# Kernel optimization log

Measured on AMD Instinct MI355X. Metric: run time of the kernel, lower is better.

The kernel has to match this reference:

```python
import jax, jax.numpy as jnp
import numpy as np

TOP_K = 2


def setup_inputs() -> dict:
    key = jax.random.key(0)
    k1, k2, k3, k4 = jax.random.split(key, 4)
    B, S, D, F, E = 4, 2048, 1024, 4096, 8
    return {
        "inputs": jax.random.normal(k1, (B, S, D), dtype=jnp.float32),
        "gate_w": jax.random.normal(k2, (D, E), dtype=jnp.float32) * 0.02,
        "w1": jax.random.normal(k3, (E, D, F), dtype=jnp.float32) * 0.02,
        "w2": jax.random.normal(k4, (E, F, D), dtype=jnp.float32) * 0.02,
    }


def reference(inputs, gate_w, w1, w2):
    # gate logits: [B, S, E]
    gate_logits = jnp.einsum("bsd,de->bse", inputs, gate_w)
    E = gate_logits.shape[-1]

    # router KL loss (matches F.kl_div(log(mean_prob), uniform, reduction='batchmean')):
    # kl = sum(u * (log u - log p_mean)) / E   (batchmean divides by first dim = E)
    gate_prob = jax.nn.softmax(gate_logits.astype(jnp.float32), axis=-1).astype(inputs.dtype)
    mean_prob = gate_prob.mean(axis=(0, 1))  # [E]
    u = jnp.full((E,), 1.0 / E, dtype=mean_prob.dtype)
    kl_loss = jnp.sum(u * (jnp.log(u) - jnp.log(mean_prob))) / E

    # top-k routing
    weights, selected = jax.lax.top_k(gate_logits, TOP_K)  # [B,S,k]
    prob = jax.nn.softmax(weights.astype(jnp.float32), axis=-1).astype(inputs.dtype)

    # combine weight per expert: [B,S,E]; zero for unselected experts
    onehot = jax.nn.one_hot(selected, E, dtype=prob.dtype)  # [B,S,k,E]
    combine = jnp.einsum("bsk,bske->bse", prob, onehot)

    results = jnp.zeros_like(inputs)
    for i in range(E):  # fixed small loop over experts
        h = jax.nn.silu(jnp.einsum("bsd,df->bsf", inputs, w1[i]))
        out = jnp.einsum("bsf,fd->bsd", h, w2[i])
        results = results + combine[..., i : i + 1] * out
    return (results, kl_loss)
```

## Files before the change

kernel.cpp:

```cpp
#include <hip/hip_runtime.h>
#include <hip/hip_bf16.h>
#include <cstdint>


#define N_TOK 8192
#define D_DIM 1024
#define F_DIM 4096
#define N_EXP 8
#define MB_MAX 72

#define CNT_OFF   0u
#define HOFF_OFF  64u
#define NMB_OFF   104u
#define ZPG_OFF   128u
#define MBE_OFF   256u
#define MBB_OFF   896u
#define PSUM_OFF  1536u
#define LIST_OFF  67072u
#define COEF_OFF  329216u
#define H1_OFF    1048576ull
#define XBF_OFF   1048576ull
#define W1T_OFF   18874368ull
#define W2T_OFF   (W1T_OFF + 67108864ull)
#define H2_OFF    (W2T_OFF + 67108864ull)
#define FULL_WS   (H2_OFF + 18432ull * 4096ull * 2ull)

typedef __attribute__((ext_vector_type(8))) short short8;
typedef __attribute__((ext_vector_type(4))) float f32x4;
typedef __attribute__((ext_vector_type(4))) float float4v;
typedef __attribute__((ext_vector_type(2))) unsigned int u32x2;

__device__ __forceinline__ unsigned short f2bf(float x) {
  unsigned int u = __float_as_uint(x);
  unsigned int r = (u + 0x7fffu + ((u >> 16) & 1u)) >> 16;
  return (unsigned short)r;
}

__device__ __forceinline__ void gload16(const void* g, void* l) {
  __builtin_amdgcn_global_load_lds(
      (const __attribute__((address_space(1))) void*)g,
      (__attribute__((address_space(3))) void*)l, 16, 0, 0);
}

__global__ void router_kernel(const float* __restrict__ x,
                              const float* __restrict__ gw,
                              int* __restrict__ cnt, int* __restrict__ list,
                              float* __restrict__ coef,
                              float* __restrict__ psum,
                              unsigned short* __restrict__ xbf) {
  const int wave = threadIdx.x >> 6;
  const int lane = threadIdx.x & 63;
  const int t = blockIdx.x * 4 + wave;

  __shared__ float bps[N_EXP];
  if (threadIdx.x < N_EXP) bps[threadIdx.x] = 0.f;
  __syncthreads();

  float lg[8] = {0.f, 0.f, 0.f, 0.f, 0.f, 0.f, 0.f, 0.f};
  const float* xr = x + (size_t)t * D_DIM;
  unsigned short* xbr = xbf + (size_t)t * D_DIM;
#pragma unroll
  for (int i = 0; i < 16; ++i) {
    int d = lane + i * 64;
    float xv = xr[d];
    xbr[d] = f2bf(xv);
    float4v w0 = *(const float4v*)(gw + d * 8);
    float4v w1 = *(const float4v*)(gw + d * 8 + 4);
    lg[0] = fmaf(xv, w0.x, lg[0]); lg[1] = fmaf(xv, w0.y, lg[1]);
    lg[2] = fmaf(xv, w0.z, lg[2]); lg[3] = fmaf(xv, w0.w, lg[3]);
    lg[4] = fmaf(xv, w1.x, lg[4]); lg[5] = fmaf(xv, w1.y, lg[5]);
    lg[6] = fmaf(xv, w1.z, lg[6]); lg[7] = fmaf(xv, w1.w, lg[7]);
  }
#pragma unroll
  for (int m = 32; m; m >>= 1) {
#pragma unroll
    for (int e = 0; e < 8; ++e) lg[e] += __shfl_xor(lg[e], m);
  }

  if (lane == 0) {
    float mx = lg[0];
#pragma unroll
    for (int e = 1; e < 8; ++e) mx = fmaxf(mx, lg[e]);
    float p[8], s = 0.f;
#pragma unroll
    for (int e = 0; e < 8; ++e) { p[e] = expf(lg[e] - mx); s += p[e]; }
    float inv = 1.f / s;
#pragma unroll
    for (int e = 0; e < 8; ++e) atomicAdd(&bps[e], p[e] * inv);

    int i0 = 0;
#pragma unroll
    for (int e = 1; e < 8; ++e) if (lg[e] > lg[i0]) i0 = e;
    int i1 = (i0 == 0) ? 1 : 0;
#pragma unroll
    for (int e = 0; e < 8; ++e) if (e != i1 && e != i0 && lg[e] > lg[i1]) i1 = e;
    float p0 = 1.f / (1.f + expf(lg[i1] - lg[i0]));
    float p1 = 1.f - p0;
    int s0 = atomicAdd(&cnt[i0], 1);
    list[i0 * N_TOK + s0] = t; coef[i0 * N_TOK + s0] = p0;
    int s1 = atomicAdd(&cnt[i1], 1);
    list[i1 * N_TOK + s1] = t; coef[i1 * N_TOK + s1] = p1;
  }
  __syncthreads();
  if (threadIdx.x < 8) psum[blockIdx.x * 8 + threadIdx.x] = bps[threadIdx.x];
}

__global__ void prefix_kernel(const int* __restrict__ cnt, int* __restrict__ hoff,
                              int* __restrict__ mbe, int* __restrict__ mbb,
                              int* __restrict__ nmb, int g) {
  if (threadIdx.x == 0) {
    int o = 0, gmb = 0;
    for (int e = 0; e < 8; ++e) {
      hoff[e] = o;
      int nb = (cnt[e] + g - 1) / g;
      for (int m = 0; m < nb; ++m) { mbe[gmb] = e; mbb[gmb] = m; ++gmb; }
      o += nb * g;
    }
    hoff[8] = o;
    *nmb = gmb;
  }
}

__global__ void kl_kernel(const float* __restrict__ psum, float* __restrict__ out_kl) {
  __shared__ float s[8];
  if (threadIdx.x < 8) s[threadIdx.x] = 0.f;
  __syncthreads();
  float loc[8] = {0.f, 0.f, 0.f, 0.f, 0.f, 0.f, 0.f, 0.f};
  for (int r = threadIdx.x; r < 2048; r += 256) {
#pragma unroll
    for (int e = 0; e < 8; ++e) loc[e] += psum[r * 8 + e];
  }
#pragma unroll
  for (int e = 0; e < 8; ++e) atomicAdd(&s[e], loc[e]);
  __syncthreads();
  if (threadIdx.x == 0) {
    float kl = 0.f;
#pragma unroll
    for (int e = 0; e < 8; ++e) {
      float mean = s[e] / 8192.f;
      kl += (logf(0.125f) - logf(mean));
    }
    out_kl[0] = kl * (0.125f * 0.125f);
  }
}

__global__ __launch_bounds__(256) void wtrans_kernel(
    const float* __restrict__ w, unsigned short* __restrict__ wt, int K, int N) {
  const int e = blockIdx.z;
  const int n0 = blockIdx.x * 64, k0 = blockIdx.y * 64;
  __shared__ float t[64][65];
  const float* we = w + (size_t)e * K * N;
  const int nl = threadIdx.x & 63;
  const int kl4 = threadIdx.x >> 6;
#pragma unroll
  for (int r = 0; r < 16; ++r) {
    int kl = r * 4 + kl4;
    t[kl][nl] = we[(size_t)(k0 + kl) * N + n0 + nl];
  }
  __syncthreads();
  unsigned short* wte = wt + (size_t)e * K * N;
  const int kp = (threadIdx.x & 31) * 2;
  const int nl8 = threadIdx.x >> 5;
#pragma unroll
  for (int r = 0; r < 8; ++r) {
    int n = r * 8 + nl8;
    unsigned int pk = (unsigned int)f2bf(t[kp][n]) |
                      ((unsigned int)f2bf(t[kp + 1][n]) << 16);
    *(unsigned int*)(wte + (size_t)(n0 + n) * K + k0 + kp) = pk;
  }
}

__device__ __forceinline__ short8 ld_frag(const unsigned short* base, int row_base,
                                          int k_base, int lane) {
  int row = row_base + (lane & 15);
  int byte = (row * 128 + (k_base + ((lane >> 4) << 3)) * 2) ^ ((row & 7) << 4);
  return *(const short8*)((const char*)base + byte);
}

__global__ __launch_bounds__(512, 2) void gemm1_v6(
    const unsigned short* __restrict__ xbf, const unsigned short* __restrict__ w1t,
    const int* __restrict__ cnt, const int* __restrict__ hoff,
    const int* __restrict__ mbe, const int* __restrict__ mbb,
    const int* __restrict__ nmb,
    const int* __restrict__ list, const unsigned short* __restrict__ zpage,
    unsigned short* __restrict__ h) {
  const int mb = blockIdx.y;
  if (mb >= *nmb) return;
  const int e = mbe[mb], mblk = mbb[mb], nblk = blockIdx.x;
  const int c = cnt[e];
  const int tid = threadIdx.x, lane = tid & 63, wave = tid >> 6;
  const int wm = (wave >> 1) * 64, wn = (wave & 1) * 64;

  __shared__ unsigned short As[256 * 64];
  __shared__ unsigned short Bs[128 * 64];

  const int rowb = tid >> 3;
  const int sw = (((tid & 7) ^ (rowb & 7)) << 4);
  const char* asrc[4]; int astep[4];
  const char* bsrc[2];
#pragma unroll
  for (int i = 0; i < 4; ++i) {
    int row = i * 64 + rowb;
    int slot = mblk * 256 + row;
    if (slot < c) {
      int tok = list[e * N_TOK + slot];
      asrc[i] = (const char*)(xbf + (size_t)tok * D_DIM) + sw;
      astep[i] = 128;
    } else {
      asrc[i] = (const char*)zpage + sw;
      astep[i] = 0;
    }
  }
#pragma unroll
  for (int i = 0; i < 2; ++i) {
    int row = i * 64 + rowb;
    bsrc[i] = (const char*)(w1t + ((size_t)e * F_DIM + nblk * 128 + row) * D_DIM) + sw;
  }

  f32x4 acc[4][4];
#pragma unroll
  for (int i = 0; i < 4; ++i)
#pragma unroll
    for (int j = 0; j < 4; ++j) acc[i][j] = f32x4{0.f, 0.f, 0.f, 0.f};

  for (int kc = 0; kc < 16; ++kc) {
    __syncthreads();
#pragma unroll
    for (int i = 0; i < 4; ++i) {
      gload16(asrc[i], (char*)As + i * 8192 + tid * 16);
      asrc[i] += astep[i];
    }
#pragma unroll
    for (int i = 0; i < 2; ++i) {
      gload16(bsrc[i], (char*)Bs + i * 8192 + tid * 16);
      bsrc[i] += 128;
    }
    __syncthreads();
#pragma unroll
    for (int ks = 0; ks < 2; ++ks) {
      short8 af[4], bb[4];
#pragma unroll
      for (int mf = 0; mf < 4; ++mf) af[mf] = ld_frag(As, wm + mf * 16, ks * 32, lane);
#pragma unroll
      for (int nf = 0; nf < 4; ++nf) bb[nf] = ld_frag(Bs, wn + nf * 16, ks * 32, lane);
#pragma unroll
      for (int mf = 0; mf < 4; ++mf)
#pragma unroll
        for (int nf = 0; nf < 4; ++nf)
          acc[mf][nf] = __builtin_amdgcn_mfma_f32_16x16x32_bf16(
              af[mf], bb[nf], acc[mf][nf], 0, 0, 0);
    }
  }

  const int hbase = hoff[e] + mblk * 256;
#pragma unroll
  for (int mf = 0; mf < 4; ++mf)
#pragma unroll
    for (int nf = 0; nf < 4; ++nf)
#pragma unroll
      for (int r = 0; r < 4; ++r) {
        float v = acc[mf][nf][r];
        v = v / (1.f + __expf(-v));
        int row = wm + mf * 16 + ((lane >> 4) << 2) + r;
        int col = nblk * 128 + wn + nf * 16 + (lane & 15);
        h[(size_t)(hbase + row) * F_DIM + col] = f2bf(v);
      }
}

__global__ __launch_bounds__(512, 2) void gemm2_v6(
    const unsigned short* __restrict__ h, const unsigned short* __restrict__ w2t,
    const int* __restrict__ cnt, const int* __restrict__ hoff,
    const int* __restrict__ mbe, const int* __restrict__ mbb,
    const int* __restrict__ nmb,
    const int* __restrict__ list, const float* __restrict__ coef,
    float* __restrict__ out) {
  const int mb = blockIdx.y;
  if (mb >= *nmb) return;
  const int e = mbe[mb], mblk = mbb[mb], nblk = blockIdx.x;
  const int c = cnt[e];
  const int kofs = blockIdx.z * 2048;
  const int tid = threadIdx.x, lane = tid & 63, wave = tid >> 6;
  const int wm = (wave >> 1) * 64, wn = (wave & 1) * 64;

  __shared__ unsigned short As[256 * 64];
  __shared__ unsigned short Bs[128 * 64];

  const int rowb = tid >> 3;
  const int sw = (((tid & 7) ^ (rowb & 7)) << 4);
  const int hbase = hoff[e] + mblk * 256;
  const char* asrc[4];
  const char* bsrc[2];
#pragma unroll
  for (int i = 0; i < 4; ++i) {
    int row = i * 64 + rowb;
    asrc[i] = (const char*)(h + (size_t)(hbase + row) * F_DIM + kofs) + sw;
  }
#pragma unroll
  for (int i = 0; i < 2; ++i) {
    int row = i * 64 + rowb;
    bsrc[i] = (const char*)(w2t + ((size_t)e * D_DIM + nblk * 128 + row) * F_DIM + kofs) + sw;
  }

  f32x4 acc[4][4];
#pragma unroll
  for (int i = 0; i < 4; ++i)
#pragma unroll
    for (int j = 0; j < 4; ++j) acc[i][j] = f32x4{0.f, 0.f, 0.f, 0.f};

  for (int kc = 0; kc < 32; ++kc) {
    __syncthreads();
#pragma unroll
    for (int i = 0; i < 4; ++i) {
      gload16(asrc[i], (char*)As + i * 8192 + tid * 16);
      asrc[i] += 128;
    }
#pragma unroll
    for (int i = 0; i < 2; ++i) {
      gload16(bsrc[i], (char*)Bs + i * 8192 + tid * 16);
      bsrc[i] += 128;
    }
    __syncthreads();
#pragma unroll
    for (int ks = 0; ks < 2; ++ks) {
      short8 af[4], bb[4];
#pragma unroll
      for (int mf = 0; mf < 4; ++mf) af[mf] = ld_frag(As, wm + mf * 16, ks * 32, lane);
#pragma unroll
      for (int nf = 0; nf < 4; ++nf) bb[nf] = ld_frag(Bs, wn + nf * 16, ks * 32, lane);
#pragma unroll
      for (int mf = 0; mf < 4; ++mf)
#pragma unroll
        for (int nf = 0; nf < 4; ++nf)
          acc[mf][nf] = __builtin_amdgcn_mfma_f32_16x16x32_bf16(
              af[mf], bb[nf], acc[mf][nf], 0, 0, 0);
    }
  }

#pragma unroll
  for (int mf = 0; mf < 4; ++mf) {
#pragma unroll
    for (int r = 0; r < 4; ++r) {
      int slot = mblk * 256 + wm + mf * 16 + ((lane >> 4) << 2) + r;
      if (slot < c) {
        int tok = list[e * N_TOK + slot];
        float cf = coef[e * N_TOK + slot];
#pragma unroll
        for (int nf = 0; nf < 4; ++nf) {
          int col = nblk * 128 + wn + nf * 16 + (lane & 15);
          unsafeAtomicAdd(&out[(size_t)tok * D_DIM + col], cf * acc[mf][nf][r]);
        }
      }
    }
  }
}

__global__ __launch_bounds__(256) void gemm1_v1(
    const float* __restrict__ x, const float* __restrict__ w1,
    const int* __restrict__ cnt, const int* __restrict__ hoff,
    const int* __restrict__ list, unsigned short* __restrict__ h) {
  const int e = blockIdx.z, mblk = blockIdx.y, nblk = blockIdx.x;
  const int c = cnt[e];
  if (mblk * 128 >= c) return;
  const int tid = threadIdx.x, lane = tid & 63, wave = tid >> 6;
  const int wm = (wave >> 1) * 64, wn = (wave & 1) * 64;

  __shared__ unsigned short At[128 * 64];
  __shared__ unsigned short Bt[128 * 64];
  __shared__ int toks[128];
  if (tid < 128) {
    int slot = mblk * 128 + tid;
    toks[tid] = (slot < c) ? list[e * N_TOK + slot] : -1;
  }
  __syncthreads();

  f32x4 acc[4][4];
#pragma unroll
  for (int i = 0; i < 4; ++i)
#pragma unroll
    for (int j = 0; j < 4; ++j) acc[i][j] = f32x4{0.f, 0.f, 0.f, 0.f};

  const float* w1e = w1 + (size_t)e * D_DIM * F_DIM;
  for (int kc = 0; kc < 16; ++kc) {
    __syncthreads();
#pragma unroll
    for (int it = 0; it < 8; ++it) {
      int lin = it * 256 + tid;
      int row = lin >> 4, c4 = lin & 15;
      int tok = toks[row];
      unsigned int lo = 0u, hi = 0u;
      if (tok >= 0) {
        float4v f = *(const float4v*)(x + (size_t)tok * D_DIM + kc * 64 + c4 * 4);
        lo = (unsigned int)f2bf(f.x) | ((unsigned int)f2bf(f.y) << 16);
        hi = (unsigned int)f2bf(f.z) | ((unsigned int)f2bf(f.w) << 16);
      }
      int byte = (row * 128 + c4 * 8) ^ ((row & 7) << 4);
      *(u32x2*)((char*)At + byte) = u32x2{lo, hi};
    }
#pragma unroll
    for (int it = 0; it < 16; ++it) {
      int lin = it * 256 + tid;
      int f_loc = lin & 127, dp = lin >> 7;
      int d = kc * 64 + dp * 2;
      const float* src = w1e + (size_t)d * F_DIM + nblk * 128 + f_loc;
      unsigned int pk = (unsigned int)f2bf(src[0]) |
                        ((unsigned int)f2bf(src[F_DIM]) << 16);
      int byte = (f_loc * 128 + dp * 4) ^ ((f_loc & 7) << 4);
      *(unsigned int*)((char*)Bt + byte) = pk;
    }
    __syncthreads();
#pragma unroll
    for (int ks = 0; ks < 2; ++ks) {
      short8 af[4], bb[4];
#pragma unroll
      for (int mf = 0; mf < 4; ++mf) af[mf] = ld_frag(At, wm + mf * 16, ks * 32, lane);
#pragma unroll
      for (int nf = 0; nf < 4; ++nf) bb[nf] = ld_frag(Bt, wn + nf * 16, ks * 32, lane);
#pragma unroll
      for (int mf = 0; mf < 4; ++mf)
#pragma unroll
        for (int nf = 0; nf < 4; ++nf)
          acc[mf][nf] = __builtin_amdgcn_mfma_f32_16x16x32_bf16(
              af[mf], bb[nf], acc[mf][nf], 0, 0, 0);
    }
  }

  const int hbase = hoff[e] + mblk * 128;
#pragma unroll
  for (int mf = 0; mf < 4; ++mf)
#pragma unroll
    for (int nf = 0; nf < 4; ++nf)
#pragma unroll
      for (int r = 0; r < 4; ++r) {
        float v = acc[mf][nf][r];
        v = v / (1.f + __expf(-v));
        int row = wm + mf * 16 + ((lane >> 4) << 2) + r;
        int col = nblk * 128 + wn + nf * 16 + (lane & 15);
        h[(size_t)(hbase + row) * F_DIM + col] = f2bf(v);
      }
}

__global__ __launch_bounds__(256) void gemm2_v1(
    const unsigned short* __restrict__ h, const float* __restrict__ w2,
    const int* __restrict__ cnt, const int* __restrict__ hoff,
    const int* __restrict__ list, const float* __restrict__ coef,
    float* __restrict__ out) {
  const int e = blockIdx.z, mblk = blockIdx.y, nblk = blockIdx.x;
  const int c = cnt[e];
  if (mblk * 128 >= c) return;
  const int tid = threadIdx.x, lane = tid & 63, wave = tid >> 6;
  const int wm = (wave >> 1) * 64, wn = (wave & 1) * 64;

  __shared__ unsigned short At[128 * 64];
  __shared__ unsigned short Bt[128 * 64];

  f32x4 acc[4][4];
#pragma unroll
  for (int i = 0; i < 4; ++i)
#pragma unroll
    for (int j = 0; j < 4; ++j) acc[i][j] = f32x4{0.f, 0.f, 0.f, 0.f};

  const int hbase = hoff[e] + mblk * 128;
  const float* w2e = w2 + (size_t)e * F_DIM * D_DIM;
  for (int kc = 0; kc < 64; ++kc) {
    __syncthreads();
#pragma unroll
    for (int it = 0; it < 8; ++it) {
      int lin = it * 256 + tid;
      int row = lin >> 4, c4 = lin & 15;
      u32x2 v = *(const u32x2*)(h + (size_t)(hbase + row) * F_DIM + kc * 64 + c4 * 4);
      int byte = (row * 128 + c4 * 8) ^ ((row & 7) << 4);
      *(u32x2*)((char*)At + byte) = v;
    }
#pragma unroll
    for (int it = 0; it < 16; ++it) {
      int lin = it * 256 + tid;
      int dcol = lin & 127, kp = lin >> 7;
      int k = kc * 64 + kp * 2;
      const float* src = w2e + (size_t)k * D_DIM + nblk * 128 + dcol;
      unsigned int pk = (unsigned int)f2bf(src[0]) |
                        ((unsigned int)f2bf(src[D_DIM]) << 16);
      int byte = (dcol * 128 + kp * 4) ^ ((dcol & 7) << 4);
      *(unsigned int*)((char*)Bt + byte) = pk;
    }
    __syncthreads();
#pragma unroll
    for (int ks = 0; ks < 2; ++ks) {
      short8 af[4], bb[4];
#pragma unroll
      for (int mf = 0; mf < 4; ++mf) af[mf] = ld_frag(At, wm + mf * 16, ks * 32, lane);
#pragma unroll
      for (int nf = 0; nf < 4; ++nf) bb[nf] = ld_frag(Bt, wn + nf * 16, ks * 32, lane);
#pragma unroll
      for (int mf = 0; mf < 4; ++mf)
#pragma unroll
        for (int nf = 0; nf < 4; ++nf)
          acc[mf][nf] = __builtin_amdgcn_mfma_f32_16x16x32_bf16(
              af[mf], bb[nf], acc[mf][nf], 0, 0, 0);
    }
  }

#pragma unroll
  for (int mf = 0; mf < 4; ++mf) {
#pragma unroll
    for (int r = 0; r < 4; ++r) {
      int slot = mblk * 128 + wm + mf * 16 + ((lane >> 4) << 2) + r;
      if (slot < c) {
        int tok = list[e * N_TOK + slot];
        float cf = coef[e * N_TOK + slot];
#pragma unroll
        for (int nf = 0; nf < 4; ++nf) {
          int col = nblk * 128 + wn + nf * 16 + (lane & 15);
          unsafeAtomicAdd(&out[(size_t)tok * D_DIM + col], cf * acc[mf][nf][r]);
        }
      }
    }
  }
}

extern "C" void kernel_launch(void* const* d_in, const int* in_sizes, int n_in,
                              void* d_out, int out_size, void* d_ws, size_t ws_size,
                              hipStream_t stream) {
  const float* x = (const float*)d_in[0];
  const float* gw = (const float*)d_in[1];
  const float* w1 = (const float*)d_in[2];
  const float* w2 = (const float*)d_in[3];
  float* out = (float*)d_out;
  char* ws = (char*)d_ws;

  int* cnt = (int*)(ws + CNT_OFF);
  int* hoff = (int*)(ws + HOFF_OFF);
  int* nmb = (int*)(ws + NMB_OFF);
  int* mbe = (int*)(ws + MBE_OFF);
  int* mbb = (int*)(ws + MBB_OFF);
  float* psum = (float*)(ws + PSUM_OFF);
  int* list = (int*)(ws + LIST_OFF);
  float* coef = (float*)(ws + COEF_OFF);
  unsigned short* xbf = (unsigned short*)(ws + XBF_OFF);

  const bool full = (ws_size >= FULL_WS);

  hipMemsetAsync(d_ws, 0, PSUM_OFF + 2048 * 8 * 4, stream);
  hipMemsetAsync(d_out, 0, (size_t)out_size * 4, stream);

  router_kernel<<<2048, 256, 0, stream>>>(x, gw, cnt, list, coef, psum, xbf);
  prefix_kernel<<<1, 64, 0, stream>>>(cnt, hoff, mbe, mbb, nmb, full ? 256 : 128);
  kl_kernel<<<1, 256, 0, stream>>>(psum, out + 8388608);

  if (full) {
    unsigned short* w1t = (unsigned short*)(ws + W1T_OFF);
    unsigned short* w2t = (unsigned short*)(ws + W2T_OFF);
    unsigned short* h = (unsigned short*)(ws + H2_OFF);
    const unsigned short* zpage = (const unsigned short*)(ws + ZPG_OFF);

    wtrans_kernel<<<dim3(64, 16, 8), 256, 0, stream>>>(w1, w1t, 1024, 4096);
    wtrans_kernel<<<dim3(16, 64, 8), 256, 0, stream>>>(w2, w2t, 4096, 1024);
    gemm1_v6<<<dim3(32, MB_MAX), 512, 0, stream>>>(xbf, w1t, cnt, hoff, mbe, mbb,
                                                   nmb, list, zpage, h);
    gemm2_v6<<<dim3(8, MB_MAX, 2), 512, 0, stream>>>(h, w2t, cnt, hoff, mbe, mbb,
                                                     nmb, list, coef, out);
  } else {
    unsigned short* h = (unsigned short*)(ws + H1_OFF);
    gemm1_v1<<<dim3(32, 64, 8), 256, 0, stream>>>(x, w1, cnt, hoff, list, h);
    gemm2_v1<<<dim3(8, 64, 8), 256, 0, stream>>>(h, w2, cnt, hoff, list, coef, out);
  }
}
```

Measured before the change: 878.3 us.

## Enlarge MoE expert GEMM tiles to 256x256 and reorder grid to m-block-major

```diff
diff --git a/kernel.cpp b/kernel.cpp
--- a/kernel.cpp
+++ b/kernel.cpp
@@ -177,27 +177,27 @@
   return *(const short8*)((const char*)base + byte);
 }
 
-__global__ __launch_bounds__(512, 2) void gemm1_v6(
+__global__ __launch_bounds__(512, 2) void gemm1_v7(
     const unsigned short* __restrict__ xbf, const unsigned short* __restrict__ w1t,
     const int* __restrict__ cnt, const int* __restrict__ hoff,
     const int* __restrict__ mbe, const int* __restrict__ mbb,
     const int* __restrict__ nmb,
     const int* __restrict__ list, const unsigned short* __restrict__ zpage,
     unsigned short* __restrict__ h) {
-  const int mb = blockIdx.y;
+  const int mb = blockIdx.x;
   if (mb >= *nmb) return;
-  const int e = mbe[mb], mblk = mbb[mb], nblk = blockIdx.x;
+  const int e = mbe[mb], mblk = mbb[mb], nblk = blockIdx.y;
   const int c = cnt[e];
   const int tid = threadIdx.x, lane = tid & 63, wave = tid >> 6;
-  const int wm = (wave >> 1) * 64, wn = (wave & 1) * 64;
+  const int wm = (wave >> 2) * 128, wn = (wave & 3) * 64;
 
   __shared__ unsigned short As[256 * 64];
-  __shared__ unsigned short Bs[128 * 64];
+  __shared__ unsigned short Bs[256 * 64];
 
   const int rowb = tid >> 3;
   const int sw = (((tid & 7) ^ (rowb & 7)) << 4);
   const char* asrc[4]; int astep[4];
-  const char* bsrc[2];
+  const char* bsrc[4];
 #pragma unroll
   for (int i = 0; i < 4; ++i) {
     int row = i * 64 + rowb;
@@ -210,16 +210,12 @@
       asrc[i] = (const char*)zpage + sw;
       astep[i] = 0;
     }
-  }
-#pragma unroll
-  for (int i = 0; i < 2; ++i) {
-    int row = i * 64 + rowb;
-    bsrc[i] = (const char*)(w1t + ((size_t)e * F_DIM + nblk * 128 + row) * D_DIM) + sw;
-  }
-
-  f32x4 acc[4][4];
-#pragma unroll
-  for (int i = 0; i < 4; ++i)
+    bsrc[i] = (const char*)(w1t + ((size_t)e * F_DIM + nblk * 256 + row) * D_DIM) + sw;
+  }
+
+  f32x4 acc[8][4];
+#pragma unroll
+  for (int i = 0; i < 8; ++i)
 #pragma unroll
     for (int j = 0; j < 4; ++j) acc[i][j] = f32x4{0.f, 0.f, 0.f, 0.f};
 
@@ -229,22 +225,19 @@
     for (int i = 0; i < 4; ++i) {
       gload16(asrc[i], (char*)As + i * 8192 + tid * 16);
       asrc[i] += astep[i];
-    }
-#pragma unroll
-    for (int i = 0; i < 2; ++i) {
       gload16(bsrc[i], (char*)Bs + i * 8192 + tid * 16);
       bsrc[i] += 128;
     }
     __syncthreads();
 #pragma unroll
     for (int ks = 0; ks < 2; ++ks) {
-      short8 af[4], bb[4];
-#pragma unroll
-      for (int mf = 0; mf < 4; ++mf) af[mf] = ld_frag(As, wm + mf * 16, ks * 32, lane);
+      short8 af[8], bb[4];
+#pragma unroll
+      for (int mf = 0; mf < 8; ++mf) af[mf] = ld_frag(As, wm + mf * 16, ks * 32, lane);
 #pragma unroll
       for (int nf = 0; nf < 4; ++nf) bb[nf] = ld_frag(Bs, wn + nf * 16, ks * 32, lane);
 #pragma unroll
-      for (int mf = 0; mf < 4; ++mf)
+      for (int mf = 0; mf < 8; ++mf)
 #pragma unroll
         for (int nf = 0; nf < 4; ++nf)
           acc[mf][nf] = __builtin_amdgcn_mfma_f32_16x16x32_bf16(
@@ -254,7 +247,7 @@
 
   const int hbase = hoff[e] + mblk * 256;
 #pragma unroll
-  for (int mf = 0; mf < 4; ++mf)
+  for (int mf = 0; mf < 8; ++mf)
 #pragma unroll
     for (int nf = 0; nf < 4; ++nf)
 #pragma unroll
@@ -262,48 +255,45 @@
         float v = acc[mf][nf][r];
         v = v / (1.f + __expf(-v));
         int row = wm + mf * 16 + ((lane >> 4) << 2) + r;
-        int col = nblk * 128 + wn + nf * 16 + (lane & 15);
+        int col = nblk * 256 + wn + nf * 16 + (lane & 15);
         h[(size_t)(hbase + row) * F_DIM + col] = f2bf(v);
       }
 }
 
-__global__ __launch_bounds__(512, 2) void gemm2_v6(
+__global__ __launch_bounds__(512, 2) void gemm2_v7(
     const unsigned short* __restrict__ h, const unsigned short* __restrict__ w2t,
     const int* __restrict__ cnt, const int* __restrict__ hoff,
     const int* __restrict__ mbe, const int* __restrict__ mbb,
     const int* __restrict__ nmb,
     const int* __restrict__ list, const float* __restrict__ coef,
     float* __restrict__ out) {
-  const int mb = blockIdx.y;
+  const int mb = blockIdx.x;
   if (mb >= *nmb) return;
-  const int e = mbe[mb], mblk = mbb[mb], nblk = blockIdx.x;
+  const int e = mbe[mb], mblk = mbb[mb];
+  const int nblk = blockIdx.y & 3;
+  const int kofs = (blockIdx.y >> 2) * 2048;
   const int c = cnt[e];
-  const int kofs = blockIdx.z * 2048;
   const int tid = threadIdx.x, lane = tid & 63, wave = tid >> 6;
-  const int wm = (wave >> 1) * 64, wn = (wave & 1) * 64;
+  const int wm = (wave >> 2) * 128, wn = (wave & 3) * 64;
 
   __shared__ unsigned short As[256 * 64];
-  __shared__ unsigned short Bs[128 * 64];
+  __shared__ unsigned short Bs[256 * 64];
 
   const int rowb = tid >> 3;
   const int sw = (((tid & 7) ^ (rowb & 7)) << 4);
   const int hbase = hoff[e] + mblk * 256;
   const char* asrc[4];
-  const char* bsrc[2];
+  const char* bsrc[4];
 #pragma unroll
   for (int i = 0; i < 4; ++i) {
     int row = i * 64 + rowb;
     asrc[i] = (const char*)(h + (size_t)(hbase + row) * F_DIM + kofs) + sw;
-  }
-#pragma unroll
-  for (int i = 0; i < 2; ++i) {
-    int row = i * 64 + rowb;
-    bsrc[i] = (const char*)(w2t + ((size_t)e * D_DIM + nblk * 128 + row) * F_DIM + kofs) + sw;
-  }
-
-  f32x4 acc[4][4];
-#pragma unroll
-  for (int i = 0; i < 4; ++i)
+    bsrc[i] = (const char*)(w2t + ((size_t)e * D_DIM + nblk * 256 + row) * F_DIM + kofs) + sw;
+  }
+
+  f32x4 acc[8][4];
+#pragma unroll
+  for (int i = 0; i < 8; ++i)
 #pragma unroll
     for (int j = 0; j < 4; ++j) acc[i][j] = f32x4{0.f, 0.f, 0.f, 0.f};
 
@@ -313,22 +303,19 @@
     for (int i = 0; i < 4; ++i) {
       gload16(asrc[i], (char*)As + i * 8192 + tid * 16);
       asrc[i] += 128;
-    }
-#pragma unroll
-    for (int i = 0; i < 2; ++i) {
       gload16(bsrc[i], (char*)Bs + i * 8192 + tid * 16);
       bsrc[i] += 128;
     }
     __syncthreads();
 #pragma unroll
     for (int ks = 0; ks < 2; ++ks) {
-      short8 af[4], bb[4];
-#pragma unroll
-      for (int mf = 0; mf < 4; ++mf) af[mf] = ld_frag(As, wm + mf * 16, ks * 32, lane);
+      short8 af[8], bb[4];
+#pragma unroll
+      for (int mf = 0; mf < 8; ++mf) af[mf] = ld_frag(As, wm + mf * 16, ks * 32, lane);
 #pragma unroll
       for (int nf = 0; nf < 4; ++nf) bb[nf] = ld_frag(Bs, wn + nf * 16, ks * 32, lane);
 #pragma unroll
-      for (int mf = 0; mf < 4; ++mf)
+      for (int mf = 0; mf < 8; ++mf)
 #pragma unroll
         for (int nf = 0; nf < 4; ++nf)
           acc[mf][nf] = __builtin_amdgcn_mfma_f32_16x16x32_bf16(
@@ -337,7 +324,7 @@
   }
 
 #pragma unroll
-  for (int mf = 0; mf < 4; ++mf) {
+  for (int mf = 0; mf < 8; ++mf) {
 #pragma unroll
     for (int r = 0; r < 4; ++r) {
       int slot = mblk * 256 + wm + mf * 16 + ((lane >> 4) << 2) + r;
@@ -346,7 +333,7 @@
         float cf = coef[e * N_TOK + slot];
 #pragma unroll
         for (int nf = 0; nf < 4; ++nf) {
-          int col = nblk * 128 + wn + nf * 16 + (lane & 15);
+          int col = nblk * 256 + wn + nf * 16 + (lane & 15);
           unsafeAtomicAdd(&out[(size_t)tok * D_DIM + col], cf * acc[mf][nf][r]);
         }
       }
@@ -554,10 +541,10 @@
 
     wtrans_kernel<<<dim3(64, 16, 8), 256, 0, stream>>>(w1, w1t, 1024, 4096);
     wtrans_kernel<<<dim3(16, 64, 8), 256, 0, stream>>>(w2, w2t, 4096, 1024);
-    gemm1_v6<<<dim3(32, MB_MAX), 512, 0, stream>>>(xbf, w1t, cnt, hoff, mbe, mbb,
+    gemm1_v7<<<dim3(MB_MAX, 16), 512, 0, stream>>>(xbf, w1t, cnt, hoff, mbe, mbb,
                                                    nmb, list, zpage, h);
-    gemm2_v6<<<dim3(8, MB_MAX, 2), 512, 0, stream>>>(h, w2t, cnt, hoff, mbe, mbb,
-                                                     nmb, list, coef, out);
+    gemm2_v7<<<dim3(MB_MAX, 8), 512, 0, stream>>>(h, w2t, cnt, hoff, mbe, mbb,
+                                                  nmb, list, coef, out);
   } else {
     unsigned short* h = (unsigned short*)(ws + H1_OFF);
     gemm1_v1<<<dim3(32, 64, 8), 256, 0, stream>>>(x, w1, cnt, hoff, list, h);
```

After: 880.9 us. Within noise of the previous version (+0.3%).
